# Kernel tuning notes

Hardware: AMD Instinct MI355X
Metric: run time of the kernel (lower is better)

## Reference

```python
import jax, jax.numpy as jnp
import numpy as np

GROUPSIZE = 128
ZERO_POINT = 8  # (maxq + 1) // 2 with maxq = 2**4 - 1


def setup_inputs() -> dict:
    key = jax.random.key(0)
    kA, ks, kq = jax.random.split(key, 3)
    M, K, N = 4096, 4096, 4096
    A = jax.random.normal(kA, (M, K), dtype=jnp.float32)
    # per-group scales, positive and small like real quantization scales
    s = jax.random.uniform(ks, (K // GROUPSIZE, N), dtype=jnp.float32) * 0.02 + 1e-3
    # int4 weights in [0, 15], packed 8 nibbles per int32 word along n
    nib = jax.random.randint(kq, (K, N), 0, 16, dtype=jnp.int32).astype(jnp.uint32)
    shifts = (4 * jnp.arange(8, dtype=jnp.uint32))
    q_u = (nib.reshape(K, N // 8, 8) << shifts).sum(axis=-1)  # uint32 (K, N//8)
    q = jax.lax.bitcast_convert_type(q_u, jnp.int32)
    return {"A": A, "s": s, "q": q}


def reference(A, s, q):
    # Unpack 8 int4 nibbles per int32 word: (K, N//8) -> (K, N)
    shifts = 4 * jnp.arange(8, dtype=jnp.int32)
    nib = (q[:, :, None] >> shifts) & 0xF  # (K, N//8, 8)
    nib = nib.reshape(q.shape[0], -1)      # (K, N)
    # Symmetric dequant with zero-point 8 and per-group (groupsize=128 rows) scales
    w = (nib.astype(A.dtype) - ZERO_POINT) * jnp.repeat(s.astype(A.dtype), GROUPSIZE, axis=0)
    return A @ w  # (M, N)
```

## Files before the change

### kernel.cpp

```cpp
#include <hip/hip_runtime.h>
#include <stdint.h>

#define GM 4096
#define GN 4096
#define GK 4096
#define QW (GN/8)

typedef __attribute__((ext_vector_type(4))) int   i32x4;
typedef __attribute__((ext_vector_type(8))) short bf16x8;
typedef __attribute__((ext_vector_type(4))) float f32x4;

#define AS1 __attribute__((address_space(1)))
#define AS3 __attribute__((address_space(3)))

static __device__ __forceinline__ void glds16(const void* g, void* l) {
  __builtin_amdgcn_global_load_lds((const AS1 uint32_t*)g, (AS3 uint32_t*)l, 16, 0, 0);
}

static __device__ __forceinline__ uint32_t bf16pack_rn(float hi, float lo) {
  uint32_t h = __float_as_uint(hi) + 0x8000u;
  uint32_t l = __float_as_uint(lo) + 0x8000u;
  return __builtin_amdgcn_perm(h, l, 0x07060302u);
}

static __device__ __forceinline__ uint32_t pack4i8(int b0, int b1, int b2, int b3) {
  return ((uint32_t)b0 & 255u) | (((uint32_t)b1 & 255u) << 8) |
         (((uint32_t)b2 & 255u) << 16) | (((uint32_t)b3 & 255u) << 24);
}

__global__ void __launch_bounds__(256) prep(const float* __restrict__ A,
                                            const float* __restrict__ S,
                                            const uint32_t* __restrict__ Q,
                                            int8_t* __restrict__ Ai,
                                            float* __restrict__ ascale,
                                            int8_t* __restrict__ Wt,
                                            float* __restrict__ wscale) {
  __shared__ uint32_t T32[128 * 32];
  __shared__ float4   red[8][32];
  __shared__ float    winv_l[128];

  const int b   = blockIdx.x;
  const int tid = threadIdx.x;

  if (b < 1024) {
    const int lane = tid & 63;
    const int row  = b * 4 + (tid >> 6);
    const float* src = A + (size_t)row * GK;
    float4 v[16];
    float m = 0.f;
    #pragma unroll
    for (int i = 0; i < 16; ++i) {
      v[i] = *(const float4*)(src + i * 256 + lane * 4);
      m = fmaxf(m, fmaxf(fmaxf(fabsf(v[i].x), fabsf(v[i].y)),
                         fmaxf(fabsf(v[i].z), fabsf(v[i].w))));
    }
    #pragma unroll
    for (int off = 32; off >= 1; off >>= 1)
      m = fmaxf(m, __shfl_xor(m, off, 64));
    const float rmax = fmaxf(m, 1e-20f);
    const float inv  = 127.0f / rmax;
    #pragma unroll
    for (int i = 0; i < 16; ++i) {
      uint32_t bb = pack4i8((int)__builtin_rintf(v[i].x * inv),
                            (int)__builtin_rintf(v[i].y * inv),
                            (int)__builtin_rintf(v[i].z * inv),
                            (int)__builtin_rintf(v[i].w * inv));
      *(uint32_t*)(Ai + (size_t)row * GK + i * 256 + lane * 4) = bb;
    }
    if (lane == 0) ascale[row] = rmax * (1.0f / 127.0f);
  } else if (b < 2048) {
    const int wb = b - 1024;
    const int n0 = (wb & 31) * 128;
    const int k0 = (wb >> 5) * 128;
    const int g  = wb >> 5;
    const int w  = tid & 15;
    const int kb = tid >> 4;

    {
      const int c4 = tid & 31;
      const int g8 = tid >> 5;
      float4 m4 = make_float4(0.f, 0.f, 0.f, 0.f);
      #pragma unroll
      for (int gg = 0; gg < 4; ++gg) {
        float4 sv = *(const float4*)(S + (size_t)(g8 * 4 + gg) * GN + n0 + c4 * 4);
        m4.x = fmaxf(m4.x, sv.x); m4.y = fmaxf(m4.y, sv.y);
        m4.z = fmaxf(m4.z, sv.z); m4.w = fmaxf(m4.w, sv.w);
      }
      red[g8][c4] = m4;
      __syncthreads();
      if (g8 == 0) {
        float4 m = red[0][c4];
        #pragma unroll
        for (int rr = 1; rr < 8; ++rr) {
          float4 o = red[rr][c4];
          m.x = fmaxf(m.x, o.x); m.y = fmaxf(m.y, o.y);
          m.z = fmaxf(m.z, o.z); m.w = fmaxf(m.w, o.w);
        }
        winv_l[c4 * 4 + 0] = 127.0f / (8.0f * m.x);
        winv_l[c4 * 4 + 1] = 127.0f / (8.0f * m.y);
        winv_l[c4 * 4 + 2] = 127.0f / (8.0f * m.z);
        winv_l[c4 * 4 + 3] = 127.0f / (8.0f * m.w);
      }
      __syncthreads();
    }

    float r[8], c[8];
    {
      const float* sp = S + (size_t)g * GN + n0 + w * 8;
      float4 sa = *(const float4*)sp, sb = *(const float4*)(sp + 4);
      float4 ia = *(const float4*)&winv_l[w * 8];
      float4 ib = *(const float4*)&winv_l[w * 8 + 4];
      const float sv[8] = {sa.x, sa.y, sa.z, sa.w, sb.x, sb.y, sb.z, sb.w};
      const float iv[8] = {ia.x, ia.y, ia.z, ia.w, ib.x, ib.y, ib.z, ib.w};
      #pragma unroll
      for (int j = 0; j < 8; ++j) { r[j] = sv[j] * iv[j]; c[j] = -8.0f * r[j]; }
    }

    const int swz = 4 * (w & 7);
    #pragma unroll
    for (int c2 = 0; c2 < 2; ++c2) {
      uint32_t q[4];
      #pragma unroll
      for (int i = 0; i < 4; ++i)
        q[i] = Q[(size_t)(k0 + c2 * 64 + kb * 4 + i) * QW + (n0 >> 3) + w];
      const int kword = c2 * 16 + kb;
      #pragma unroll
      for (int j = 0; j < 8; ++j) {
        int bb[4];
        #pragma unroll
        for (int i = 0; i < 4; ++i) {
          float nib = (float)((q[i] >> (4 * j)) & 0xFu);
          bb[i] = (int)__builtin_rintf(fmaf(nib, r[j], c[j]));
        }
        T32[(w * 8 + j) * 32 + (kword ^ swz)] = pack4i8(bb[0], bb[1], bb[2], bb[3]);
      }
    }
    __syncthreads();
    #pragma unroll
    for (int p = 0; p < 4; ++p) {
      int idx = p * 256 + tid;
      int n = idx >> 3, gr = idx & 7;
      uint4 v = *(const uint4*)(&T32[n * 32 + (gr ^ ((n >> 3) & 7)) * 4]);
      *(uint4*)(Wt + (size_t)(n0 + n) * GK + k0 + gr * 16) = v;
    }
  } else {
    const int n = (b - 2048) * 256 + tid;
    float m = 0.f;
    #pragma unroll 8
    for (int gg = 0; gg < 32; ++gg) m = fmaxf(m, S[(size_t)gg * GN + n]);
    wscale[n] = m * (8.0f / 127.0f);
  }
}

__global__ void __launch_bounds__(512, 4) gemm_i8(const int8_t* __restrict__ Ai,
                                                  const int8_t* __restrict__ Wi,
                                                  const float* __restrict__ ascale,
                                                  const float* __restrict__ wscale,
                                                  float* __restrict__ C) {
  __shared__ __align__(16) int8_t As[3][64 * 128];
  __shared__ __align__(16) int8_t Bs[3][128 * 128];

  const int tid = threadIdx.x;
  const int bid = blockIdx.y * gridDim.x + blockIdx.x;
  const int swb = ((bid & 7) << 6) | (bid >> 3);
  const int m0  = (swb >> 4) * 128;
  const int n0  = (swb & 15) * 256;

  const int lane = tid & 63;
  const int wid  = tid >> 6;
  const int wm   = wid >> 2;
  const int wn   = wid & 3;
  const int col  = lane & 15;
  const int quad = lane >> 4;

  const int sline = tid >> 3;
  const int sphys = tid & 7;
  const int sl    = sphys ^ (sline & 7);
  const int arow  = 2 * sline + (sl >> 2);
  const int kcs   = (sl & 3) << 4;
  const int8_t* Asrc  = Ai + (size_t)(m0 + arow) * GK + kcs;
  const int8_t* Bsrc  = Wi + (size_t)(n0 + arow) * GK + kcs;
  const int8_t* Bsrc2 = Bsrc + (size_t)128 * GK;

#define STAGE(b, ko) do {                                    \
    glds16(Asrc  + (ko), &As[b][tid * 16]);                  \
    glds16(Bsrc  + (ko), &Bs[b][tid * 16]);                  \
    glds16(Bsrc2 + (ko), &Bs[b][8192 + tid * 16]);           \
  } while (0)

  const int phq = (((col & 1) << 2) | quad) ^ (col >> 1);
  const int aRd = (wm * 32 + (col >> 1)) * 128 + phq * 16;
  const int bRd = (wn * 32 + (col >> 1)) * 128 + phq * 16;

  i32x4 af[4], bf[4];
  i32x4 acc[4][4];
  #pragma unroll
  for (int i = 0; i < 4; ++i)
    #pragma unroll
    for (int j = 0; j < 4; ++j)
      acc[i][j] = (i32x4){0, 0, 0, 0};

#define LD_(b) do {                                                   \
    _Pragma("unroll")                                                 \
    for (int x_ = 0; x_ < 4; ++x_) {                                  \
      af[x_] = *(const i32x4*)(&As[b][aRd + x_ * 1024]);              \
      bf[x_] = *(const i32x4*)(&Bs[b][bRd + x_ * 1024]);              \
    }                                                                 \
  } while (0)
#define MFMA16_() do {                                                \
    _Pragma("unroll")                                                 \
    for (int m_ = 0; m_ < 4; ++m_)                                    \
      _Pragma("unroll")                                               \
      for (int n_ = 0; n_ < 4; ++n_)                                  \
        acc[m_][n_] = __builtin_amdgcn_mfma_i32_16x16x64_i8(          \
            af[m_], bf[n_], acc[m_][n_], 0, 0, 0);                    \
  } while (0)
#define VM3()   asm volatile("s_waitcnt vmcnt(3)" ::: "memory")
#define BARM()  asm volatile("s_barrier" ::: "memory")
#define PRIO1() __builtin_amdgcn_s_setprio(1)
#define PRIO0() __builtin_amdgcn_s_setprio(0)

#define STEP(B_CUR, B_NXT, KO_NXT) do {                               \
    VM3();                               \
    BARM();                            \
    STAGE(B_NXT, (KO_NXT));       \
    LD_(B_CUR);                                                       \
    PRIO1(); MFMA16_(); PRIO0();                                      \
  } while (0)

  STAGE(0, 0);
  STAGE(1, 64);

  for (int it = 0; it < 21; ++it) {
    const int t = 3 * it;
    STEP(0, 2, ((t + 2) & 63) << 6);
    STEP(1, 0, ((t + 3) & 63) << 6);
    STEP(2, 1, ((t + 4) & 63) << 6);
  }
  VM3();
  BARM();
  LD_(0);
  PRIO1(); MFMA16_(); PRIO0();

  #pragma unroll
  for (int mt = 0; mt < 4; ++mt) {
    const int rbase = m0 + wm * 64 + mt * 16 + quad * 4;
    float4 a4 = *(const float4*)(ascale + rbase);
    const float ar[4] = {a4.x, a4.y, a4.z, a4.w};
    #pragma unroll
    for (int nt = 0; nt < 4; ++nt) {
      const int cbase = n0 + wn * 64 + nt * 16 + col;
      const float ws = wscale[cbase];
      #pragma unroll
      for (int r = 0; r < 4; ++r)
        C[(size_t)(rbase + r) * GN + cbase]
          = (float)acc[mt][nt][r] * (ar[r] * ws);
    }
  }
#undef STAGE
#undef LD_
#undef MFMA16_
#undef VM3
#undef BARM
#undef PRIO1
#undef PRIO0
#undef STEP
}

#define BM 128
#define BN 128
#define BK 32

__global__ void __launch_bounds__(256) w4a32_gemm(
    const float* __restrict__ A,
    const float* __restrict__ S,
    const uint32_t* __restrict__ Q,
    float* __restrict__ C)
{
  __shared__ __align__(16) ushort As[BM*BK];
  __shared__ __align__(16) ushort Bs[BN*BK];

  const int tid  = threadIdx.x;
  const int m0   = blockIdx.y*BM;
  const int n0   = blockIdx.x*BN;
  const int wcol  = tid & 15;
  const int kpair = tid >> 4;
  const int ln   = tid & 63;
  const int wid  = tid >> 6;
  const int wm   = (wid >> 1) * 64;
  const int wn   = (wid & 1) * 64;
  const int col  = ln & 15;
  const int quad = ln >> 4;

  f32x4 acc[4][4];
  #pragma unroll
  for (int i=0;i<4;++i)
    #pragma unroll
    for (int j=0;j<4;++j)
      acc[i][j] = (f32x4){0.f,0.f,0.f,0.f};

  float sv[8], cv[8];
  float4 spf0, spf1;

  const float*    Abase = A + (size_t)m0 * GK;
  const uint32_t* Qbase = Q + (size_t)(n0>>3) + wcol;

  {
    const float* sp = S + n0 + wcol*8;
    spf0 = *(const float4*)sp;
    spf1 = *(const float4*)(sp + 4);
  }

  float4 a4[4];
  uint32_t wqa, wqb;
  #pragma unroll
  for (int i=0;i<4;++i) {
    int f = tid + i*256;
    a4[i] = *(const float4*)(Abase + (size_t)(f>>3)*GK + ((f&7)*4));
  }
  wqa = Qbase[(size_t)(2*kpair)   * QW];
  wqb = Qbase[(size_t)(2*kpair+1) * QW];

  for (int k0 = 0; k0 < GK; k0 += BK) {
    if ((k0 & 127) == 0) {
      sv[0]=spf0.x; sv[1]=spf0.y; sv[2]=spf0.z; sv[3]=spf0.w;
      sv[4]=spf1.x; sv[5]=spf1.y; sv[6]=spf1.z; sv[7]=spf1.w;
      #pragma unroll
      for (int j=0;j<8;++j) cv[j] = -8.0f * sv[j];
    }

    #pragma unroll
    for (int i=0;i<4;++i) {
      int f = tid + i*256;
      int row = f>>3, c4 = f&7;
      *(uint2*)(&As[row*BK + c4*4]) =
        make_uint2(bf16pack_rn(a4[i].y, a4[i].x), bf16pack_rn(a4[i].w, a4[i].z));
    }

    {
      const int kk = (2*kpair) ^ (8*(wcol&3));
      #pragma unroll
      for (int j=0;j<8;++j) {
        float fa = (float)((wqa >> (4*j)) & 0xFu);
        float fb = (float)((wqb >> (4*j)) & 0xFu);
        float wa = fmaf(fa, sv[j], cv[j]);
        float wb = fmaf(fb, sv[j], cv[j]);
        int n = wcol*8 + j;
        *(uint32_t*)(&Bs[n*BK + kk]) = bf16pack_rn(wb, wa);
      }
    }

    int kn = k0 + BK; if (kn >= GK) kn = 0;
    if ((kn & 127) == 0) {
      const float* sp = S + (size_t)(kn>>7)*GN + n0 + wcol*8;
      spf0 = *(const float4*)sp;
      spf1 = *(const float4*)(sp + 4);
    }
    #pragma unroll
    for (int i=0;i<4;++i) {
      int f = tid + i*256;
      a4[i] = *(const float4*)(Abase + (size_t)(f>>3)*GK + kn + ((f&7)*4));
    }
    wqa = Qbase[(size_t)(kn + 2*kpair)   * QW];
    wqb = Qbase[(size_t)(kn + 2*kpair+1) * QW];

    __syncthreads();

    bf16x8 af[4], bfr[4];
    #pragma unroll
    for (int t=0;t<4;++t) {
      af[t] = *(const bf16x8*)(&As[(wm + t*16 + col)*BK + quad*8]);
      int n = wn + t*16 + col;
      int kk = (quad*8) ^ (8*((n>>3)&3));
      bfr[t] = *(const bf16x8*)(&Bs[n*BK + kk]);
    }
    #pragma unroll
    for (int mt=0;mt<4;++mt)
      #pragma unroll
      for (int nt=0;nt<4;++nt)
        acc[mt][nt] = __builtin_amdgcn_mfma_f32_16x16x32_bf16(
                          af[mt], bfr[nt], acc[mt][nt], 0, 0, 0);

    __syncthreads();
  }

  #pragma unroll
  for (int mt=0;mt<4;++mt)
    #pragma unroll
    for (int nt=0;nt<4;++nt)
      #pragma unroll
      for (int r=0;r<4;++r)
        C[(size_t)(m0 + wm + mt*16 + quad*4 + r)*GN + n0 + wn + nt*16 + col]
          = acc[mt][nt][r];
}

extern "C" void kernel_launch(void* const* d_in, const int* in_sizes, int n_in,
                              void* d_out, int out_size, void* d_ws, size_t ws_size,
                              hipStream_t stream) {
  const float*    A = (const float*)d_in[0];
  const float*    S = (const float*)d_in[1];
  const uint32_t* Q = (const uint32_t*)d_in[2];
  float*          C = (float*)d_out;

  const size_t need = (size_t)GM * GK + (size_t)GN * GK + 3 * 4096 * 4 + 4096;
  if (ws_size >= need) {
    int8_t* Ai  = (int8_t*)d_ws;
    int8_t* Wt  = Ai + (size_t)GM * GK;
    float* ascale = (float*)(Wt + (size_t)GN * GK);
    float* wscale = ascale + 4096;
    prep<<<dim3(1024 + 1024 + 16), dim3(256), 0, stream>>>(A, S, Q, Ai, ascale, Wt, wscale);
    gemm_i8<<<dim3(16, 32), dim3(512), 0, stream>>>(Ai, Wt, ascale, wscale, C);
  } else {
    w4a32_gemm<<<dim3(GN / BN, GM / BM), dim3(256), 0, stream>>>(A, S, Q, C);
  }
}
```

Baseline: 192.8 us.

## Prepack weights in MFMA fragment layout and load B directly to registers

The prep kernel now writes int8 weights in a fragment-major layout matching the MFMA B-operand, so each lane's 16 bytes are contiguous. The GEMM drops the LDS staging for B and loads B fragments straight from global memory into double-buffered registers, while A keeps a four-deep LDS ring. This is meant to cut LDS traffic, LDS footprint and barrier pressure for B. In exchange, waves that share B columns now each fetch them from global/L2, and one out-of-range prefetch happens on the last step.

```diff
diff --git a/kernel.cpp b/kernel.cpp
--- a/kernel.cpp
+++ b/kernel.cpp
@@ -33,7 +33,7 @@
                                             const uint32_t* __restrict__ Q,
                                             int8_t* __restrict__ Ai,
                                             float* __restrict__ ascale,
-                                            int8_t* __restrict__ Wt,
+                                            int8_t* __restrict__ Bf,
                                             float* __restrict__ wscale) {
   __shared__ uint32_t T32[128 * 32];
   __shared__ float4   red[8][32];
@@ -136,12 +136,21 @@
       }
     }
     __syncthreads();
-    #pragma unroll
-    for (int p = 0; p < 4; ++p) {
-      int idx = p * 256 + tid;
-      int n = idx >> 3, gr = idx & 7;
-      uint4 v = *(const uint4*)(&T32[n * 32 + (gr ^ ((n >> 3) & 7)) * 4]);
-      *(uint4*)(Wt + (size_t)(n0 + n) * GK + k0 + gr * 16) = v;
+    {
+      const int l16 = tid & 63;
+      const int sub = tid >> 6;
+      #pragma unroll
+      for (int p = 0; p < 4; ++p) {
+        const int d     = p * 4 + sub;
+        const int n16l  = d >> 1;
+        const int kcl   = d & 1;
+        const int col_l = n16l * 16 + (l16 & 15);
+        const int gr    = (kcl << 2) | ((l16 >> 4) & 3);
+        uint4 v = *(const uint4*)(&T32[col_l * 32 + ((gr ^ ((col_l >> 3) & 7)) << 2)]);
+        const size_t n16g = (size_t)((n0 >> 4) + n16l);
+        const size_t kcg  = (size_t)((k0 >> 6) + kcl);
+        *(uint4*)(Bf + (((n16g << 6) + kcg) << 10) + (l16 << 4)) = v;
+      }
     }
   } else {
     const int n = (b - 2048) * 256 + tid;
@@ -153,12 +162,11 @@
 }
 
 __global__ void __launch_bounds__(512, 4) gemm_i8(const int8_t* __restrict__ Ai,
-                                                  const int8_t* __restrict__ Wi,
+                                                  const int8_t* __restrict__ Bf,
                                                   const float* __restrict__ ascale,
                                                   const float* __restrict__ wscale,
                                                   float* __restrict__ C) {
-  __shared__ __align__(16) int8_t As[3][64 * 128];
-  __shared__ __align__(16) int8_t Bs[3][128 * 128];
+  __shared__ __align__(16) int8_t As[4][64 * 128];
 
   const int tid = threadIdx.x;
   const int bid = blockIdx.y * gridDim.x + blockIdx.x;
@@ -178,21 +186,15 @@
   const int sl    = sphys ^ (sline & 7);
   const int arow  = 2 * sline + (sl >> 2);
   const int kcs   = (sl & 3) << 4;
-  const int8_t* Asrc  = Ai + (size_t)(m0 + arow) * GK + kcs;
-  const int8_t* Bsrc  = Wi + (size_t)(n0 + arow) * GK + kcs;
-  const int8_t* Bsrc2 = Bsrc + (size_t)128 * GK;
-
-#define STAGE(b, ko) do {                                    \
-    glds16(Asrc  + (ko), &As[b][tid * 16]);                  \
-    glds16(Bsrc  + (ko), &Bs[b][tid * 16]);                  \
-    glds16(Bsrc2 + (ko), &Bs[b][8192 + tid * 16]);           \
-  } while (0)
+  const int8_t* Asrc = Ai + (size_t)(m0 + arow) * GK + kcs;
+
+  const int n16b = (n0 >> 4) + wn * 4;
+  const int8_t* Bp = Bf + ((size_t)n16b << 16) + (lane << 4);
 
   const int phq = (((col & 1) << 2) | quad) ^ (col >> 1);
   const int aRd = (wm * 32 + (col >> 1)) * 128 + phq * 16;
-  const int bRd = (wn * 32 + (col >> 1)) * 128 + phq * 16;
-
-  i32x4 af[4], bf[4];
+
+  i32x4 af[4], bfr[2][4];
   i32x4 acc[4][4];
   #pragma unroll
   for (int i = 0; i < 4; ++i)
@@ -200,47 +202,51 @@
     for (int j = 0; j < 4; ++j)
       acc[i][j] = (i32x4){0, 0, 0, 0};
 
-#define LD_(b) do {                                                   \
-    _Pragma("unroll")                                                 \
-    for (int x_ = 0; x_ < 4; ++x_) {                                  \
-      af[x_] = *(const i32x4*)(&As[b][aRd + x_ * 1024]);              \
-      bf[x_] = *(const i32x4*)(&Bs[b][bRd + x_ * 1024]);              \
-    }                                                                 \
+#define STAGE(b, ko) glds16(Asrc + (ko), &As[b][tid * 16])
+#define LDBF(s, kc) do {                                                     \
+    _Pragma("unroll")                                                        \
+    for (int n_ = 0; n_ < 4; ++n_)                                           \
+      bfr[s][n_] = *(const i32x4*)(Bp + ((size_t)n_ << 16)                   \
+                                      + ((size_t)(kc) << 10));               \
   } while (0)
-#define MFMA16_() do {                                                \
-    _Pragma("unroll")                                                 \
-    for (int m_ = 0; m_ < 4; ++m_)                                    \
-      _Pragma("unroll")                                               \
-      for (int n_ = 0; n_ < 4; ++n_)                                  \
-        acc[m_][n_] = __builtin_amdgcn_mfma_i32_16x16x64_i8(          \
-            af[m_], bf[n_], acc[m_][n_], 0, 0, 0);                    \
+#define LDA_(b) do {                                                         \
+    _Pragma("unroll")                                                        \
+    for (int x_ = 0; x_ < 4; ++x_)                                           \
+      af[x_] = *(const i32x4*)(&As[b][aRd + x_ * 1024]);                     \
   } while (0)
-#define VM3()   asm volatile("s_waitcnt vmcnt(3)" ::: "memory")
+#define MFMA16_(s) do {                                                      \
+    _Pragma("unroll")                                                        \
+    for (int m_ = 0; m_ < 4; ++m_)                                           \
+      _Pragma("unroll")                                                      \
+      for (int n_ = 0; n_ < 4; ++n_)                                         \
+        acc[m_][n_] = __builtin_amdgcn_mfma_i32_16x16x64_i8(                 \
+            af[m_], bfr[s][n_], acc[m_][n_], 0, 0, 0);                       \
+  } while (0)
+#define VMW()   asm volatile("s_waitcnt vmcnt(1)" ::: "memory")
 #define BARM()  asm volatile("s_barrier" ::: "memory")
 #define PRIO1() __builtin_amdgcn_s_setprio(1)
 #define PRIO0() __builtin_amdgcn_s_setprio(0)
 
-#define STEP(B_CUR, B_NXT, KO_NXT) do {                               \
-    VM3();                               \
-    BARM();                            \
-    STAGE(B_NXT, (KO_NXT));       \
-    LD_(B_CUR);                                                       \
-    PRIO1(); MFMA16_(); PRIO0();                                      \
+#define STEP(T) do {                                                         \
+    VMW();                           \
+    BARM();                           \
+    LDBF((T) + 1 < 64 ? ((T)+1) & 1 : 0, (T) + 1);         \
+    STAGE(((T) + 2) & 3, (((T) + 2) & 63) << 6);          \
+    LDA_((T) & 3);                                                           \
+    PRIO1(); MFMA16_((T) & 1); PRIO0();                                      \
   } while (0)
 
   STAGE(0, 0);
+  LDBF(0, 0);
   STAGE(1, 64);
 
-  for (int it = 0; it < 21; ++it) {
-    const int t = 3 * it;
-    STEP(0, 2, ((t + 2) & 63) << 6);
-    STEP(1, 0, ((t + 3) & 63) << 6);
-    STEP(2, 1, ((t + 4) & 63) << 6);
-  }
-  VM3();
-  BARM();
-  LD_(0);
-  PRIO1(); MFMA16_(); PRIO0();
+  for (int it = 0; it < 16; ++it) {
+    const int t = it * 4;
+    STEP(t + 0);
+    STEP(t + 1);
+    STEP(t + 2);
+    STEP(t + 3);
+  }
 
   #pragma unroll
   for (int mt = 0; mt < 4; ++mt) {
@@ -258,9 +264,10 @@
     }
   }
 #undef STAGE
-#undef LD_
+#undef LDBF
+#undef LDA_
 #undef MFMA16_
-#undef VM3
+#undef VMW
 #undef BARM
 #undef PRIO1
 #undef PRIO0
@@ -405,11 +412,11 @@
   const size_t need = (size_t)GM * GK + (size_t)GN * GK + 3 * 4096 * 4 + 4096;
   if (ws_size >= need) {
     int8_t* Ai  = (int8_t*)d_ws;
-    int8_t* Wt  = Ai + (size_t)GM * GK;
-    float* ascale = (float*)(Wt + (size_t)GN * GK);
+    int8_t* Bfr = Ai + (size_t)GM * GK;
+    float* ascale = (float*)(Bfr + (size_t)GN * GK);
     float* wscale = ascale + 4096;
-    prep<<<dim3(1024 + 1024 + 16), dim3(256), 0, stream>>>(A, S, Q, Ai, ascale, Wt, wscale);
-    gemm_i8<<<dim3(16, 32), dim3(512), 0, stream>>>(Ai, Wt, ascale, wscale, C);
+    prep<<<dim3(1024 + 1024 + 16), dim3(256), 0, stream>>>(A, S, Q, Ai, ascale, Bfr, wscale);
+    gemm_i8<<<dim3(16, 32), dim3(512), 0, stream>>>(Ai, Bfr, ascale, wscale, C);
   } else {
     w4a32_gemm<<<dim3(GN / BN, GM / BM), dim3(256), 0, stream>>>(A, S, Q, C);
   }
```

Result: no change. 196.6 us (+2.0%).
